# Optimization experiments

Hardware: AMD Instinct MI355X
Metric: run time of the kernel (lower is better)

The kernel has to match this reference:

```python
import jax, jax.numpy as jnp
import numpy as np

NUM_HEADS = 6
ATTN_TH = 0.0
NEG_INF = -10000.0  # masked-score fill for threshold pruning


def setup_inputs() -> dict:
    key = jax.random.key(0)
    k1, k2, k3 = jax.random.split(key, 3)
    B, N, C = 8, 1024, 384
    x = jax.random.normal(k1, (B, N, C), dtype=jnp.float32)
    # Linear weights (torch layout: [out, in]), scaled like default init
    w_qkv = jax.random.normal(k2, (3 * C, C), dtype=jnp.float32) * (1.0 / np.sqrt(C))
    b_qkv = jnp.zeros((3 * C,), dtype=jnp.float32)
    w_proj = jax.random.normal(k3, (C, C), dtype=jnp.float32) * (1.0 / np.sqrt(C))
    b_proj = jnp.zeros((C,), dtype=jnp.float32)
    return {"x": x, "w_qkv": w_qkv, "b_qkv": b_qkv, "w_proj": w_proj, "b_proj": b_proj}


def reference(x, w_qkv, b_qkv, w_proj, b_proj):
    B, N, C = x.shape
    H = NUM_HEADS
    D = C // H
    scale = D ** -0.5
    # QAct nodes are identity (quant=False); QLinear is a plain linear.
    qkv = jnp.einsum('bnc,oc->bno', x, w_qkv) + b_qkv          # [B,N,3C]
    qkv = qkv.reshape(B, N, 3, H, D).transpose(2, 0, 3, 1, 4)   # [3,B,H,N,D]
    q, k, v = qkv[0], qkv[1], qkv[2]
    attn = jnp.einsum('bhnd,bhmd->bhnm', q, k) * scale          # [B,H,N,N]
    # Threshold pruning: scores below Attn_Th are masked out of the softmax.
    attn = jnp.where(attn < ATTN_TH, NEG_INF, attn)
    attn = jax.nn.softmax(attn, axis=-1)
    out = jnp.einsum('bhnm,bhmd->bhnd', attn, v)                # [B,H,N,D]
    out = out.transpose(0, 2, 1, 3).reshape(B, N, C)
    out = jnp.einsum('bnc,oc->bno', out, w_proj) + b_proj
    return out
```

## Files before the change

kernel.cpp:

```cpp
#include <hip/hip_runtime.h>
#include <hip/hip_bf16.h>


typedef __attribute__((__ext_vector_type__(8))) __bf16 bf16x8;
typedef __attribute__((__ext_vector_type__(8))) unsigned short ushort8;
typedef __attribute__((__ext_vector_type__(4))) unsigned short ushort4v;
typedef __attribute__((__ext_vector_type__(4))) short short4v;
typedef __attribute__((__ext_vector_type__(4))) float f32x4;

#define NX 3145728
#define NQ 442368
#define NP 147456

__device__ __forceinline__ f32x4 mfma32(bf16x8 a, bf16x8 b, f32x4 c) {
    return __builtin_amdgcn_mfma_f32_16x16x32_bf16(a, b, c, 0, 0, 0);
}
__device__ __forceinline__ f32x4 mfma16(short4v a, short4v b, f32x4 c) {
    return __builtin_amdgcn_mfma_f32_16x16x16bf16_1k(a, b, c, 0, 0, 0);
}

__device__ __forceinline__ unsigned short f2bf(float f) {
    union { float f; unsigned int i; } x; x.f = f;
    unsigned int u = x.i;
    return (unsigned short)((u + 0x7fffu + ((u >> 16) & 1u)) >> 16);
}

__device__ __forceinline__ void dma16(const unsigned short* g, unsigned short* l) {
    __builtin_amdgcn_global_load_lds(
        (const __attribute__((address_space(1))) unsigned int*)g,
        (__attribute__((address_space(3))) unsigned int*)l, 16, 0, 0);
}

__global__ __launch_bounds__(256) void cvt_bf16(
    const float* __restrict__ x, const float* __restrict__ wq, const float* __restrict__ wp,
    unsigned short* __restrict__ xb, unsigned short* __restrict__ wqb, unsigned short* __restrict__ wpb)
{
    int i = blockIdx.x * 256 + threadIdx.x;
    const float* src; unsigned short* dst; int off;
    if (i < NX / 4)              { src = x;  dst = xb;  off = i * 4; }
    else if (i < (NX + NQ) / 4)  { src = wq; dst = wqb; off = i * 4 - NX; }
    else                         { src = wp; dst = wpb; off = i * 4 - NX - NQ; }
    float4 v = *(const float4*)(src + off);
    ushort4v r;
    r[0] = f2bf(v.x); r[1] = f2bf(v.y); r[2] = f2bf(v.z); r[3] = f2bf(v.w);
    *(ushort4v*)(dst + off) = r;
}

template <int MODE, int TM>
__global__ __launch_bounds__(TM * 2) void gemm_bt(
    const unsigned short* __restrict__ A,
    const unsigned short* __restrict__ B,
    const float* __restrict__ bias,
    unsigned short* __restrict__ qg,
    unsigned short* __restrict__ kg,
    unsigned short* __restrict__ vg,
    float* __restrict__ out,
    int M, int N, int K)
{
    const int tid  = threadIdx.x;
    const int lane = tid & 63;
    const int wave = tid >> 6;
    const int l15  = lane & 15;
    const int quad = lane >> 4;
    const int m0 = blockIdx.x * TM;
    const int n0 = blockIdx.y * 128;
    const int wm = (wave >> 1) * 64;
    const int wn = (wave & 1) * 64;

    __shared__ __align__(16) unsigned short As[2 * TM * 32];
    __shared__ __align__(16) unsigned short Bs[2 * 128 * 32];

    f32x4 acc[4][4];
    #pragma unroll
    for (int i = 0; i < 4; ++i)
        #pragma unroll
        for (int j = 0; j < 4; ++j)
            acc[i][j] = (f32x4){0.f, 0.f, 0.f, 0.f};

    auto stage = [&](int k0, int buf) {
        #pragma unroll
        for (int t = 0; t < 2; ++t) {
            int i = tid + t * TM * 2;
            dma16(A + (size_t)(m0 + (i >> 2)) * K + k0 + (i & 3) * 8,
                  As + buf * TM * 32 + t * TM * 16 + wave * 512);
        }
        #pragma unroll
        for (int t = 0; t < 512 / (TM * 2); ++t) {
            int i = tid + t * TM * 2;
            dma16(B + (size_t)(n0 + (i >> 2)) * K + k0 + (i & 3) * 8,
                  Bs + buf * 4096 + t * TM * 16 + wave * 512);
        }
    };

    const int nk = K >> 5;
    stage(0, 0);
    for (int ki = 0; ki < nk; ++ki) {
        __syncthreads();
        if (ki + 1 < nk) stage((ki + 1) << 5, (ki + 1) & 1);
        const unsigned short* as = As + (ki & 1) * TM * 32;
        const unsigned short* bs = Bs + (ki & 1) * 4096;

        bf16x8 af[4], bff[4];
        #pragma unroll
        for (int mt = 0; mt < 4; ++mt)
            af[mt] = *(const bf16x8*)(as + (wm + mt * 16 + l15) * 32 + quad * 8);
        #pragma unroll
        for (int nt = 0; nt < 4; ++nt)
            bff[nt] = *(const bf16x8*)(bs + (wn + nt * 16 + l15) * 32 + quad * 8);
        #pragma unroll
        for (int mt = 0; mt < 4; ++mt)
            #pragma unroll
            for (int nt = 0; nt < 4; ++nt)
                acc[mt][nt] = mfma32(af[mt], bff[nt], acc[mt][nt]);
    }

    if constexpr (MODE == 0) {
        if (n0 < 384) {
            #pragma unroll
            for (int nt = 0; nt < 4; ++nt) {
                int n = n0 + wn + nt * 16 + l15;
                float bv = bias[n];
                #pragma unroll
                for (int mt = 0; mt < 4; ++mt) {
                    int mbase = m0 + wm + mt * 16 + quad * 4;
                    #pragma unroll
                    for (int r = 0; r < 4; ++r)
                        qg[(size_t)(mbase + r) * 384 + n] = f2bf((acc[mt][nt][r] + bv) * 0.125f);
                }
            }
        } else if (n0 < 768) {
            #pragma unroll
            for (int nt = 0; nt < 4; ++nt) {
                int n = n0 + wn + nt * 16 + l15;
                float bv = bias[n];
                int c2 = n - 384;
                int h = c2 >> 6, ck = c2 & 63;
                int half = ck >> 5, qd = (ck >> 3) & 3, j = ck & 7;
                #pragma unroll
                for (int mt = 0; mt < 4; ++mt) {
                    int mbase = m0 + wm + mt * 16 + quad * 4;
                    #pragma unroll
                    for (int r = 0; r < 4; ++r) {
                        int tok = mbase + r;
                        int b = tok >> 10, kv = tok & 1023;
                        int kt = kv >> 4, lk = kv & 15;
                        kg[(size_t)(b * 6 + h) * 65536 +
                           ((((size_t)kt * 2 + half) * 4 + qd) * 16 + lk) * 8 + j]
                            = f2bf(acc[mt][nt][r] + bv);
                    }
                }
            }
        } else {
            #pragma unroll
            for (int nt = 0; nt < 4; ++nt) {
                int n = n0 + wn + nt * 16 + l15;
                float bv = bias[n];
                int c2 = n - 768;
                int h = c2 >> 6, d = c2 & 63;
                int dt = d >> 4, lv = d & 15;
                #pragma unroll
                for (int mt = 0; mt < 4; ++mt) {
                    int mbase = m0 + wm + mt * 16 + quad * 4;
                    int b = mbase >> 10, kvb = mbase & 1023;
                    int cc = kvb >> 6, jt = (kvb >> 4) & 3, qd = (kvb >> 2) & 3;
                    ushort4v pk;
                    #pragma unroll
                    for (int r = 0; r < 4; ++r) pk[r] = f2bf(acc[mt][nt][r] + bv);
                    *(ushort4v*)(vg + (size_t)(b * 6 + h) * 65536 + (size_t)cc * 4096 +
                                 (((jt * 4 + dt) * 4 + qd) * 16 + lv) * 4) = pk;
                }
            }
        }
    } else {
        #pragma unroll
        for (int nt = 0; nt < 4; ++nt) {
            int n = n0 + wn + nt * 16 + l15;
            float bv = bias[n];
            #pragma unroll
            for (int mt = 0; mt < 4; ++mt) {
                int mbase = m0 + wm + mt * 16 + quad * 4;
                #pragma unroll
                for (int r = 0; r < 4; ++r)
                    out[(size_t)(mbase + r) * N + n] = acc[mt][nt][r] + bv;
            }
        }
    }
}

__global__ __launch_bounds__(256) void attn_fused(
    const unsigned short* __restrict__ qg,
    const unsigned short* __restrict__ kg,
    const unsigned short* __restrict__ vg,
    unsigned short* __restrict__ aout)
{
    const int tid  = threadIdx.x;
    const int wave = tid >> 6;
    const int lane = tid & 63;
    const int l15  = lane & 15;
    const int quad = lane >> 4;
    const int id = blockIdx.x;
    const int s  = id % 48;
    const int qt = id / 48;
    const int b  = s / 6;
    const int h  = s % 6;

    const size_t rowbase = (size_t)b * 1024;
    const unsigned short* Kslab = kg + (size_t)s * 65536;
    const unsigned short* Vslab = vg + (size_t)s * 65536;
    const int q0 = qt * 64 + wave * 16;

    __shared__ __align__(16) unsigned short Kb[2 * 4096];
    __shared__ __align__(16) unsigned short Vb[2 * 4096];

    bf16x8 aq0, aq1;
    {
        const unsigned short* qrow = qg + (rowbase + q0 + l15) * 384 + h * 64 + quad * 8;
        aq0 = *(const bf16x8*)qrow;
        aq1 = *(const bf16x8*)(qrow + 32);
    }

    f32x4 accO[4];
    #pragma unroll
    for (int dt = 0; dt < 4; ++dt) accO[dt] = (f32x4){0.f, 0.f, 0.f, 0.f};
    float lsum = 0.f;

    auto stage = [&](int c, int buf) {
        #pragma unroll
        for (int t = 0; t < 2; ++t) {
            int i = tid + t * 256;
            dma16(Kslab + (size_t)c * 4096 + i * 8, Kb + buf * 4096 + t * 2048 + wave * 512);
            dma16(Vslab + (size_t)c * 4096 + i * 8, Vb + buf * 4096 + t * 2048 + wave * 512);
        }
    };

    stage(0, 0);
    for (int c = 0; c < 16; ++c) {
        __syncthreads();
        if (c + 1 < 16) stage(c + 1, (c + 1) & 1);
        const unsigned short* kb = Kb + (c & 1) * 4096;
        const unsigned short* vb = Vb + (c & 1) * 4096;

        #pragma unroll
        for (int kt = 0; kt < 4; ++kt) {
            bf16x8 ka = *(const bf16x8*)(kb + (((kt * 2 + 0) * 4 + quad) * 16 + l15) * 8);
            bf16x8 kbf = *(const bf16x8*)(kb + (((kt * 2 + 1) * 4 + quad) * 16 + l15) * 8);
            f32x4 z = (f32x4){0.f, 0.f, 0.f, 0.f};
            z = mfma32(ka, aq0, z);
            z = mfma32(kbf, aq1, z);

            short4v p;
            #pragma unroll
            for (int r = 0; r < 4; ++r) {
                float sc = z[r];
                sc = (sc < 0.f) ? 0.f : __expf(sc);
                lsum += sc;
                p[r] = (short)f2bf(sc);
            }
            #pragma unroll
            for (int dt = 0; dt < 4; ++dt) {
                short4v vv = *(const short4v*)(vb + (((kt * 4 + dt) * 4 + quad) * 16 + l15) * 4);
                accO[dt] = mfma16(vv, p, accO[dt]);
            }
        }
    }

    lsum += __shfl_xor(lsum, 16, 64);
    lsum += __shfl_xor(lsum, 32, 64);
    float inv = 1.0f / lsum;

    unsigned short* orow = aout + (rowbase + q0 + l15) * 384 + h * 64 + quad * 4;
    #pragma unroll
    for (int dt = 0; dt < 4; ++dt) {
        ushort4v pk;
        #pragma unroll
        for (int r = 0; r < 4; ++r) pk[r] = f2bf(accO[dt][r] * inv);
        *(ushort4v*)(orow + dt * 16) = pk;
    }
}

extern "C" void kernel_launch(void* const* d_in, const int* in_sizes, int n_in,
                              void* d_out, int out_size, void* d_ws, size_t ws_size,
                              hipStream_t stream) {
    const float* x      = (const float*)d_in[0];
    const float* w_qkv  = (const float*)d_in[1];
    const float* b_qkv  = (const float*)d_in[2];
    const float* w_proj = (const float*)d_in[3];
    const float* b_proj = (const float*)d_in[4];
    float* out = (float*)d_out;

    unsigned short* qg   = (unsigned short*)d_ws;
    unsigned short* kgp  = qg   + (size_t)NX;
    unsigned short* vgp  = kgp  + (size_t)NX;
    unsigned short* aout = vgp  + (size_t)NX;
    unsigned short* xb   = aout + (size_t)NX;
    unsigned short* wqb  = xb   + (size_t)NX;
    unsigned short* wpb  = wqb  + (size_t)NQ;

    cvt_bf16<<<3648, 256, 0, stream>>>(x, w_qkv, w_proj, xb, wqb, wpb);
    gemm_bt<0, 256><<<dim3(32, 9), 512, 0, stream>>>(
        xb, wqb, b_qkv, qg, kgp, vgp, nullptr, 8192, 1152, 384);
    attn_fused<<<768, 256, 0, stream>>>(qg, kgp, vgp, aout);
    gemm_bt<1, 128><<<dim3(64, 3), 256, 0, stream>>>(
        aout, wpb, b_proj, nullptr, nullptr, nullptr, out, 8192, 384, 384);
}
```

Before: 128.9 us.

## Streamline attention softmax with exp2, packed bf16 converts and MFMA row sums

```diff
diff --git a/kernel.cpp b/kernel.cpp
--- a/kernel.cpp
+++ b/kernel.cpp
@@ -12,6 +12,8 @@
 #define NQ 442368
 #define NP 147456
 
+#define QSCALE 0.1803368801111204f
+
 __device__ __forceinline__ f32x4 mfma32(bf16x8 a, bf16x8 b, f32x4 c) {
     return __builtin_amdgcn_mfma_f32_16x16x32_bf16(a, b, c, 0, 0, 0);
 }
@@ -23,6 +25,12 @@
     union { float f; unsigned int i; } x; x.f = f;
     unsigned int u = x.i;
     return (unsigned short)((u + 0x7fffu + ((u >> 16) & 1u)) >> 16);
+}
+
+__device__ __forceinline__ unsigned cvtpk(float a, float b) {
+    unsigned r;
+    asm("v_cvt_pk_bf16_f32 %0, %1, %2" : "=v"(r) : "v"(a), "v"(b));
+    return r;
 }
 
 __device__ __forceinline__ void dma16(const unsigned short* g, unsigned short* l) {
@@ -125,7 +133,7 @@
                     int mbase = m0 + wm + mt * 16 + quad * 4;
                     #pragma unroll
                     for (int r = 0; r < 4; ++r)
-                        qg[(size_t)(mbase + r) * 384 + n] = f2bf((acc[mt][nt][r] + bv) * 0.125f);
+                        qg[(size_t)(mbase + r) * 384 + n] = f2bf((acc[mt][nt][r] + bv) * QSCALE);
                 }
             }
         } else if (n0 < 768) {
@@ -219,10 +227,12 @@
         aq1 = *(const bf16x8*)(qrow + 32);
     }
 
+    const short4v ONES4 = (short4v){(short)0x3F80, (short)0x3F80, (short)0x3F80, (short)0x3F80};
+
     f32x4 accO[4];
     #pragma unroll
     for (int dt = 0; dt < 4; ++dt) accO[dt] = (f32x4){0.f, 0.f, 0.f, 0.f};
-    float lsum = 0.f;
+    f32x4 accS = (f32x4){0.f, 0.f, 0.f, 0.f};
 
     auto stage = [&](int c, int buf) {
         #pragma unroll
@@ -248,14 +258,17 @@
             z = mfma32(ka, aq0, z);
             z = mfma32(kbf, aq1, z);
 
-            short4v p;
-            #pragma unroll
-            for (int r = 0; r < 4; ++r) {
-                float sc = z[r];
-                sc = (sc < 0.f) ? 0.f : __expf(sc);
-                lsum += sc;
-                p[r] = (short)f2bf(sc);
-            }
+            float e0 = __builtin_amdgcn_exp2f(z[0]); e0 = (z[0] < 0.f) ? 0.f : e0;
+            float e1 = __builtin_amdgcn_exp2f(z[1]); e1 = (z[1] < 0.f) ? 0.f : e1;
+            float e2 = __builtin_amdgcn_exp2f(z[2]); e2 = (z[2] < 0.f) ? 0.f : e2;
+            float e3 = __builtin_amdgcn_exp2f(z[3]); e3 = (z[3] < 0.f) ? 0.f : e3;
+
+            union { unsigned u[2]; short4v s; } pp;
+            pp.u[0] = cvtpk(e0, e1);
+            pp.u[1] = cvtpk(e2, e3);
+            short4v p = pp.s;
+
+            accS = mfma16(ONES4, p, accS);
             #pragma unroll
             for (int dt = 0; dt < 4; ++dt) {
                 short4v vv = *(const short4v*)(vb + (((kt * 4 + dt) * 4 + quad) * 16 + l15) * 4);
@@ -264,17 +277,15 @@
         }
     }
 
-    lsum += __shfl_xor(lsum, 16, 64);
-    lsum += __shfl_xor(lsum, 32, 64);
-    float inv = 1.0f / lsum;
+    float inv = 1.0f / accS[0];
 
     unsigned short* orow = aout + (rowbase + q0 + l15) * 384 + h * 64 + quad * 4;
     #pragma unroll
     for (int dt = 0; dt < 4; ++dt) {
-        ushort4v pk;
-        #pragma unroll
-        for (int r = 0; r < 4; ++r) pk[r] = f2bf(accO[dt][r] * inv);
-        *(ushort4v*)(orow + dt * 16) = pk;
+        union { unsigned u[2]; ushort4v s; } pk;
+        pk.u[0] = cvtpk(accO[dt][0] * inv, accO[dt][1] * inv);
+        pk.u[1] = cvtpk(accO[dt][2] * inv, accO[dt][3] * inv);
+        *(ushort4v*)(orow + dt * 16) = pk.s;
     }
 }
 
@@ -300,6 +311,6 @@
     gemm_bt<0, 256><<<dim3(32, 9), 512, 0, stream>>>(
         xb, wqb, b_qkv, qg, kgp, vgp, nullptr, 8192, 1152, 384);
     attn_fused<<<768, 256, 0, stream>>>(qg, kgp, vgp, aout);
-    gemm_bt<1, 128><<<dim3(64, 3), 256, 0, stream>>>(
+    gemm_bt<1, 64><<<dim3(128, 3), 128, 0, stream>>>(
         aout, wpb, b_proj, nullptr, nullptr, nullptr, out, 8192, 384, 384);
 }
```

After: 124.0 us. 1.04x faster.
